# Kernel tuning notes

Measured on AMD Instinct MI355X. Metric: run time of the kernel, lower is better.

## Reference

```python
import jax, jax.numpy as jnp
import numpy as np

W, B, C, H = 1600, 4, 1, 900
DENSITY = 0.03          # fraction of valid radar returns per column
DEPTH_MAX = 80.0        # metric depth range


def setup_inputs() -> dict:
    key = jax.random.key(0)
    k1, k2, k3 = jax.random.split(key, 3)
    radar_depth = jax.random.uniform(k1, (W, B, C, H, 1), jnp.float32) * DEPTH_MAX + 1.0
    radar_mask = jax.random.uniform(k2, (W, B, C, H, 1), jnp.float32) < DENSITY
    radar_patches = jnp.where(radar_mask, radar_depth, 0.0)
    # dense monocular depth estimate, strictly positive (all 'valid')
    mde_out_patches = jax.random.uniform(k3, (W, B, C, H, 1), jnp.float32) * DEPTH_MAX + 1.0
    return {"radar_patches": radar_patches, "mde_out_patches": mde_out_patches}


def _process_column(radar_col, mde_col):
    """Sequentially place valid radar depths of one (w,b) column.

    radar_col, mde_col: [H] float (channel 0 of the column).
    Returns radar_gt column [H].
    Matches torch loop: for each valid radar y (ascending), pick mde row with
    closest depth (argmin |mde - d|, first index on ties); if that slot is
    already occupied, search outward offsets +1,-1,+2,-2,... for an empty slot;
    if none found, overwrite the best slot.
    """
    h = radar_col.shape[0]
    ys = jnp.arange(h)
    mde_valid = mde_col != 0
    has_mde = jnp.any(mde_valid)
    BIG = jnp.float32(1e30)
    KBIG = 4 * h  # sentinel key for occupied slots

    def step(col, y):
        depth = radar_col[y]
        valid = depth != 0
        # per-point argmin over valid mde depths
        diffs = jnp.where(mde_valid, jnp.abs(mde_col - depth), BIG)
        best_y = jnp.where(has_mde, jnp.argmin(diffs), y)
        # outward collision search as a vectorized argmin over a priority key:
        #   best_y itself -> 0; offset o, +dy before -dy -> 2*o + (dy<0)
        occ = col != 0
        dy = ys - best_y
        key = 2 * jnp.abs(dy) + (dy < 0).astype(jnp.int32)
        key = jnp.where(ys == best_y, 0, key)
        key = jnp.where(occ, KBIG, key)
        final_y = jnp.argmin(key)
        # all slots occupied -> fall back to best_y (torch overwrites there)
        final_y = jnp.where(key[final_y] >= KBIG, best_y, final_y)
        new_col = jnp.where(valid, col.at[final_y].set(depth), col)
        return new_col, None

    col, _ = jax.lax.scan(step, jnp.zeros(h, radar_col.dtype), ys)
    return col


def reference(radar_patches, mde_out_patches):
    # channel 0 only is read/written, as in the torch code
    radar0 = radar_patches[:, :, 0, :, 0]   # [W, B, H]
    mde0 = mde_out_patches[:, :, 0, :, 0]   # [W, B, H]
    cols = jax.vmap(jax.vmap(_process_column))(radar0, mde0)  # [W, B, H]
    w, b, h = cols.shape
    c = radar_patches.shape[2]
    radar_gt = jnp.zeros((b, c, h, w), radar_patches.dtype)
    radar_gt = radar_gt.at[:, 0].set(jnp.transpose(cols, (1, 2, 0)))  # [B, H, W]
    return radar_gt
```

## Files before the change

### kernel.cpp

```cpp
#include <hip/hip_runtime.h>
#include <cstdint>
#include <cstddef>

#define WDIM 1600
#define BDIM 4
#define HDIM 900
#define NV4  225
#define QCAP 96
#define KBIG (4 * HDIM)
#define BW   6

#define DPP_MINF(v, ctrl)                                                  \
    v = fminf(v, __int_as_float(__builtin_amdgcn_update_dpp(               \
            __float_as_int(v), __float_as_int(v), ctrl, 0xf, 0xf, false)))

__global__ __launch_bounds__(64) void radar_place_kernel(
    const float* __restrict__ radar, const float* __restrict__ mde,
    float* __restrict__ colout , int direct, float* __restrict__ out)
{
    __shared__ __align__(16) float s_col[HDIM];
    __shared__ float s_qd[QCAP];
    __shared__ int   s_qy[QCAP];

    const int lane = threadIdx.x;
    const int colid = blockIdx.x;
    const float4* mde4   = (const float4*)mde   + (long)colid * NV4;
    const float4* radar4 = (const float4*)radar + (long)colid * NV4;
    float4* col4 = (float4*)s_col;

    const unsigned long long below = (1ull << lane) - 1ull;

    bool hm = false;
#pragma unroll
    for (int c = 0; c < 4; ++c) {
        int i4 = c * 64 + lane;
        if (i4 < NV4) {
            float4 mv = mde4[i4];
            hm = hm || (mv.x != 0.f) || (mv.y != 0.f) || (mv.z != 0.f) || (mv.w != 0.f);
            col4[i4] = mv;
        }
    }
    const bool has_mde = (__ballot(hm) != 0ull);

    int Q = 0;
#pragma unroll
    for (int c = 0; c < 4; ++c) {
        int i4 = c * 64 + lane;
        bool in = (i4 < NV4);
        float4 rv = in ? radar4[i4] : make_float4(0.f, 0.f, 0.f, 0.f);
        unsigned long long b0 = __ballot(rv.x != 0.f);
        unsigned long long b1 = __ballot(rv.y != 0.f);
        unsigned long long b2 = __ballot(rv.z != 0.f);
        unsigned long long b3 = __ballot(rv.w != 0.f);
        int pos = Q + __popcll(b0 & below) + __popcll(b1 & below)
                    + __popcll(b2 & below) + __popcll(b3 & below);
        int y0 = i4 * 4;
        if (rv.x != 0.f) { if (pos < QCAP) { s_qd[pos] = rv.x; s_qy[pos] = y0;     } pos++; }
        if (rv.y != 0.f) { if (pos < QCAP) { s_qd[pos] = rv.y; s_qy[pos] = y0 + 1; } pos++; }
        if (rv.z != 0.f) { if (pos < QCAP) { s_qd[pos] = rv.z; s_qy[pos] = y0 + 2; } pos++; }
        if (rv.w != 0.f) { if (pos < QCAP) { s_qd[pos] = rv.w; s_qy[pos] = y0 + 3; } pos++; }
        Q += __popcll(b0) + __popcll(b1) + __popcll(b2) + __popcll(b3);
    }
    if (Q > QCAP) Q = QCAP;

    __syncthreads();

    float m[15];
    if (lane < 60) {
        int yb = lane * 15;
#pragma unroll
        for (int k = 0; k < 15; ++k) {
            float v = s_col[yb + k];
            m[k] = (v != 0.f) ? v : 1e30f;
        }
    } else {
#pragma unroll
        for (int k = 0; k < 15; ++k) m[k] = 1e30f;
    }

    __syncthreads();

#pragma unroll
    for (int c = 0; c < 4; ++c) {
        int i4 = c * 64 + lane;
        if (i4 < NV4) col4[i4] = make_float4(0.f, 0.f, 0.f, 0.f);
    }

    unsigned occ = (lane >= 60) ? 0x7FFFu : 0u;

    for (int t = 0; t < Q; t += BW) {
        float d[BW];
#pragma unroll
        for (int i = 0; i < BW; ++i) {
            int idx = (t + i < Q) ? (t + i) : (Q - 1);
            d[i] = s_qd[idx];
        }
        float bd[BW], bo[BW];
        int bik[BW];
#pragma unroll
        for (int i = 0; i < BW; ++i) { bd[i] = 3.4e38f; bik[i] = 0; }
#pragma unroll
        for (int k = 0; k < 15; ++k) {
            float mm = m[k];
#pragma unroll
            for (int i = 0; i < BW; ++i) {
                float af = fabsf(mm - d[i]);
                if (af < bd[i]) { bd[i] = af; bik[i] = k; }
            }
        }
#pragma unroll
        for (int i = 0; i < BW; ++i) bo[i] = bd[i];
#pragma unroll
        for (int i = 0; i < BW; ++i) DPP_MINF(bd[i], 0x111);
#pragma unroll
        for (int i = 0; i < BW; ++i) DPP_MINF(bd[i], 0x112);
#pragma unroll
        for (int i = 0; i < BW; ++i) DPP_MINF(bd[i], 0x114);
#pragma unroll
        for (int i = 0; i < BW; ++i) DPP_MINF(bd[i], 0x118);
#pragma unroll
        for (int i = 0; i < BW; ++i) DPP_MINF(bd[i], 0x142);
#pragma unroll
        for (int i = 0; i < BW; ++i) DPP_MINF(bd[i], 0x143);

#pragma unroll
        for (int i = 0; i < BW; ++i) {
            if (t + i < Q) {
                int best;
                if (has_mde) {
                    float gm = __int_as_float(
                        __builtin_amdgcn_readlane(__float_as_int(bd[i]), 63));
                    unsigned long long wm = __ballot(bo[i] == gm);
                    int win = __ffsll((long long)wm) - 1;
                    int kst = __shfl(bik[i], win);
                    best = win * 15 + kst;
                } else {
                    best = s_qy[t + i];
                }
                float depth = d[i];
                int sb = __builtin_amdgcn_readfirstlane(best);
                int bl = sb / 15, bk = sb % 15;
                unsigned long long bm = __ballot((occ >> bk) & 1u);
                int final_y = sb;
                if ((bm >> bl) & 1ull) {
                    int ko = 0x7fffffff, kk = 0;
#pragma unroll
                    for (int k = 0; k < 15; ++k) {
                        int yy = lane * 15 + k;
                        int o = (occ >> k) & 1;
                        int dy = yy - sb;
                        int ad = dy < 0 ? -dy : dy;
                        int key = o ? KBIG : (2 * ad + (dy < 0 ? 1 : 0));
                        if (key < ko) { ko = key; kk = k; }
                    }
                    int kmin = ko;
#pragma unroll
                    for (int off = 32; off; off >>= 1) {
                        int v = __shfl_xor(kmin, off);
                        kmin = (v < kmin) ? v : kmin;
                    }
                    if (kmin < KBIG) {
                        unsigned long long wm2 = __ballot(ko == kmin);
                        int w2 = __ffsll((long long)wm2) - 1;
                        int k2 = __shfl(kk, w2);
                        final_y = w2 * 15 + k2;
                    }
                }
                int sf = __builtin_amdgcn_readfirstlane(final_y);
                int fl = sf / 15, fk = sf % 15;
                if (lane == fl) occ |= (1u << fk);
                if (lane == 0) s_col[sf] = depth;
            }
        }
    }

    __syncthreads();

    if (direct) {
        int w_ = colid >> 2, b_ = colid & 3;
#pragma unroll
        for (int c = 0; c < 4; ++c) {
            int i4 = c * 64 + lane;
            if (i4 < NV4) {
                float4 v = col4[i4];
                int y = i4 * 4;
                out[((long)(b_ * HDIM + y + 0)) * WDIM + w_] = v.x;
                out[((long)(b_ * HDIM + y + 1)) * WDIM + w_] = v.y;
                out[((long)(b_ * HDIM + y + 2)) * WDIM + w_] = v.z;
                out[((long)(b_ * HDIM + y + 3)) * WDIM + w_] = v.w;
            }
        }
    } else {
        float4* colout4 = (float4*)colout + (long)colid * NV4;
#pragma unroll
        for (int c = 0; c < 4; ++c) {
            int i4 = c * 64 + lane;
            if (i4 < NV4) colout4[i4] = col4[i4];
        }
    }
}

__global__ __launch_bounds__(256) void transpose_kernel(
    const float* __restrict__ colout, float* __restrict__ out)
{
    __shared__ float tile[32][33];
    const int b  = blockIdx.z;
    const int h0 = blockIdx.x * 32;
    const int w0 = blockIdx.y * 32;
    const int tx = threadIdx.x & 31;
    const int ty = threadIdx.x >> 5;
#pragma unroll
    for (int j = 0; j < 4; ++j) {
        int wl = ty + j * 8;
        int w = w0 + wl;
        int h = h0 + tx;
        float v = 0.0f;
        if (h < HDIM && w < WDIM) v = colout[((long)(w * BDIM + b)) * HDIM + h];
        tile[wl][tx] = v;
    }
    __syncthreads();
#pragma unroll
    for (int j = 0; j < 4; ++j) {
        int hl = ty + j * 8;
        int h = h0 + hl;
        int w = w0 + tx;
        if (h < HDIM && w < WDIM)
            out[((long)(b * HDIM + h)) * WDIM + w] = tile[tx][hl];
    }
}

extern "C" void kernel_launch(void* const* d_in, const int* in_sizes, int n_in,
                              void* d_out, int out_size, void* d_ws, size_t ws_size,
                              hipStream_t stream) {
    const float* radar = (const float*)d_in[0];
    const float* mde   = (const float*)d_in[1];
    float* out = (float*)d_out;
    float* ws  = (float*)d_ws;

    const size_t need = (size_t)WDIM * BDIM * HDIM * sizeof(float);
    const int direct = (ws_size < need) ? 1 : 0;

    hipLaunchKernelGGL(radar_place_kernel,
                       dim3(WDIM * BDIM), dim3(64), 0, stream,
                       radar, mde, ws, direct, out);

    if (!direct) {
        dim3 g((HDIM + 31) / 32, WDIM / 32, BDIM);
        hipLaunchKernelGGL(transpose_kernel, g, dim3(256), 0, stream, ws, out);
    }
}
```

Before: 137.0 us.

## Pack four columns per block and decouple argmin from serial slot placement

Each block now runs four wavefronts, one column each, with per-wave shared buffers, and the block-wide barriers are removed. The radar queue is held in registers and broadcast with readlane instead of being reread from LDS. All best-row argmins are computed first in batches, then a separate serial loop resolves slot collisions using a DPP integer min-reduction instead of shfl_xor. Final depths are scattered in parallel by each owning lane. This cuts per-step latency in the serial placement chain and the launch/occupancy overhead of 64-thread blocks. The risk is that in the all-occupied fallback, where several points may write the same slot, the write order is no longer guaranteed.

```diff
diff --git a/kernel.cpp b/kernel.cpp
--- a/kernel.cpp
+++ b/kernel.cpp
@@ -9,24 +9,37 @@
 #define QCAP 96
 #define KBIG (4 * HDIM)
 #define BW   6
+#define NWAVE 4
 
 #define DPP_MINF(v, ctrl)                                                  \
     v = fminf(v, __int_as_float(__builtin_amdgcn_update_dpp(               \
             __float_as_int(v), __float_as_int(v), ctrl, 0xf, 0xf, false)))
-
-__global__ __launch_bounds__(64) void radar_place_kernel(
+#define DPP_MINI(v, ctrl)                                                  \
+    { int _t = __builtin_amdgcn_update_dpp(v, v, ctrl, 0xf, 0xf, false);   \
+      v = _t < v ? _t : v; }
+
+__device__ __forceinline__ float rdlane_f(float v, int l) {
+    return __int_as_float(__builtin_amdgcn_readlane(__float_as_int(v), l));
+}
+
+__global__ __launch_bounds__(64 * NWAVE, 6) void radar_place_kernel(
     const float* __restrict__ radar, const float* __restrict__ mde,
     float* __restrict__ colout , int direct, float* __restrict__ out)
 {
-    __shared__ __align__(16) float s_col[HDIM];
-    __shared__ float s_qd[QCAP];
-    __shared__ int   s_qy[QCAP];
-
-    const int lane = threadIdx.x;
-    const int colid = blockIdx.x;
+    __shared__ __align__(16) float s_col[NWAVE][HDIM];
+    __shared__ float s_qd[NWAVE][QCAP];
+    __shared__ int   s_qy[NWAVE][QCAP];
+
+    const int wave = threadIdx.x >> 6;
+    const int lane = threadIdx.x & 63;
+    const int colid = blockIdx.x * NWAVE + wave;
     const float4* mde4   = (const float4*)mde   + (long)colid * NV4;
     const float4* radar4 = (const float4*)radar + (long)colid * NV4;
-    float4* col4 = (float4*)s_col;
+
+    float*  colw = s_col[wave];
+    float4* col4 = (float4*)colw;
+    float*  qd   = s_qd[wave];
+    int*    qy   = s_qy[wave];
 
     const unsigned long long below = (1ull << lane) - 1ull;
 
@@ -55,22 +68,20 @@
         int pos = Q + __popcll(b0 & below) + __popcll(b1 & below)
                     + __popcll(b2 & below) + __popcll(b3 & below);
         int y0 = i4 * 4;
-        if (rv.x != 0.f) { if (pos < QCAP) { s_qd[pos] = rv.x; s_qy[pos] = y0;     } pos++; }
-        if (rv.y != 0.f) { if (pos < QCAP) { s_qd[pos] = rv.y; s_qy[pos] = y0 + 1; } pos++; }
-        if (rv.z != 0.f) { if (pos < QCAP) { s_qd[pos] = rv.z; s_qy[pos] = y0 + 2; } pos++; }
-        if (rv.w != 0.f) { if (pos < QCAP) { s_qd[pos] = rv.w; s_qy[pos] = y0 + 3; } pos++; }
+        if (rv.x != 0.f) { if (pos < QCAP) { qd[pos] = rv.x; qy[pos] = y0;     } pos++; }
+        if (rv.y != 0.f) { if (pos < QCAP) { qd[pos] = rv.y; qy[pos] = y0 + 1; } pos++; }
+        if (rv.z != 0.f) { if (pos < QCAP) { qd[pos] = rv.z; qy[pos] = y0 + 2; } pos++; }
+        if (rv.w != 0.f) { if (pos < QCAP) { qd[pos] = rv.w; qy[pos] = y0 + 3; } pos++; }
         Q += __popcll(b0) + __popcll(b1) + __popcll(b2) + __popcll(b3);
     }
     if (Q > QCAP) Q = QCAP;
-
-    __syncthreads();
 
     float m[15];
     if (lane < 60) {
         int yb = lane * 15;
 #pragma unroll
         for (int k = 0; k < 15; ++k) {
-            float v = s_col[yb + k];
+            float v = colw[yb + k];
             m[k] = (v != 0.f) ? v : 1e30f;
         }
     } else {
@@ -78,7 +89,10 @@
         for (int k = 0; k < 15; ++k) m[k] = 1e30f;
     }
 
-    __syncthreads();
+    float dq_lo = 0.f, dq_hi = 0.f;
+    int   qy_lo = 0,   qy_hi = 0;
+    if (lane < Q)      { dq_lo = qd[lane];      qy_lo = qy[lane]; }
+    if (lane + 64 < Q) { dq_hi = qd[lane + 64]; qy_hi = qy[lane + 64]; }
 
 #pragma unroll
     for (int c = 0; c < 4; ++c) {
@@ -86,14 +100,16 @@
         if (i4 < NV4) col4[i4] = make_float4(0.f, 0.f, 0.f, 0.f);
     }
 
-    unsigned occ = (lane >= 60) ? 0x7FFFu : 0u;
-
+    int best_lo = 0, best_hi = 0;
     for (int t = 0; t < Q; t += BW) {
+        int idxs[BW];
         float d[BW];
 #pragma unroll
         for (int i = 0; i < BW; ++i) {
-            int idx = (t + i < Q) ? (t + i) : (Q - 1);
-            d[i] = s_qd[idx];
+            int idx = t + i; if (idx >= Q) idx = Q - 1;
+            idxs[i] = idx;
+            if (idx < 64) d[i] = rdlane_f(dq_lo, idx);
+            else          d[i] = rdlane_f(dq_hi, idx - 64);
         }
         float bd[BW], bo[BW];
         int bik[BW];
@@ -122,59 +138,71 @@
         for (int i = 0; i < BW; ++i) DPP_MINF(bd[i], 0x142);
 #pragma unroll
         for (int i = 0; i < BW; ++i) DPP_MINF(bd[i], 0x143);
-
 #pragma unroll
         for (int i = 0; i < BW; ++i) {
-            if (t + i < Q) {
-                int best;
-                if (has_mde) {
-                    float gm = __int_as_float(
-                        __builtin_amdgcn_readlane(__float_as_int(bd[i]), 63));
-                    unsigned long long wm = __ballot(bo[i] == gm);
-                    int win = __ffsll((long long)wm) - 1;
-                    int kst = __shfl(bik[i], win);
-                    best = win * 15 + kst;
-                } else {
-                    best = s_qy[t + i];
-                }
-                float depth = d[i];
-                int sb = __builtin_amdgcn_readfirstlane(best);
-                int bl = sb / 15, bk = sb % 15;
-                unsigned long long bm = __ballot((occ >> bk) & 1u);
-                int final_y = sb;
-                if ((bm >> bl) & 1ull) {
-                    int ko = 0x7fffffff, kk = 0;
-#pragma unroll
-                    for (int k = 0; k < 15; ++k) {
-                        int yy = lane * 15 + k;
-                        int o = (occ >> k) & 1;
-                        int dy = yy - sb;
-                        int ad = dy < 0 ? -dy : dy;
-                        int key = o ? KBIG : (2 * ad + (dy < 0 ? 1 : 0));
-                        if (key < ko) { ko = key; kk = k; }
-                    }
-                    int kmin = ko;
-#pragma unroll
-                    for (int off = 32; off; off >>= 1) {
-                        int v = __shfl_xor(kmin, off);
-                        kmin = (v < kmin) ? v : kmin;
-                    }
-                    if (kmin < KBIG) {
-                        unsigned long long wm2 = __ballot(ko == kmin);
-                        int w2 = __ffsll((long long)wm2) - 1;
-                        int k2 = __shfl(kk, w2);
-                        final_y = w2 * 15 + k2;
-                    }
-                }
-                int sf = __builtin_amdgcn_readfirstlane(final_y);
-                int fl = sf / 15, fk = sf % 15;
-                if (lane == fl) occ |= (1u << fk);
-                if (lane == 0) s_col[sf] = depth;
-            }
-        }
-    }
-
-    __syncthreads();
+            int idx = idxs[i];
+            int sb;
+            if (has_mde) {
+                float gm = rdlane_f(bd[i], 63);
+                unsigned long long wm = __ballot(bo[i] == gm);
+                int win = __ffsll((long long)wm) - 1;
+                int kst = __builtin_amdgcn_readlane(bik[i], win);
+                sb = win * 15 + kst;
+            } else {
+                if (idx < 64) sb = __builtin_amdgcn_readlane(qy_lo, idx);
+                else          sb = __builtin_amdgcn_readlane(qy_hi, idx - 64);
+            }
+            if (idx < 64) { if (lane == idx)      best_lo = sb; }
+            else          { if (lane == idx - 64) best_hi = sb; }
+        }
+    }
+
+    unsigned occ = (lane >= 60) ? 0x7FFFu : 0u;
+    int fy_lo = 0, fy_hi = 0;
+
+    auto place_one = [&](int sb) -> int {
+        int bl = sb / 15, bk = sb - bl * 15;
+        unsigned long long bm = __ballot((occ >> bk) & 1u);
+        int fy = sb;
+        if ((bm >> bl) & 1ull) {
+            int ko = 0x7fffffff, kk = 0;
+#pragma unroll
+            for (int k = 0; k < 15; ++k) {
+                int yy = lane * 15 + k;
+                int o = (occ >> k) & 1;
+                int dy = yy - sb;
+                int ad = dy < 0 ? -dy : dy;
+                int key = o ? KBIG : (2 * ad + (dy < 0 ? 1 : 0));
+                if (key < ko) { ko = key; kk = k; }
+            }
+            int km = ko;
+            DPP_MINI(km, 0x111); DPP_MINI(km, 0x112); DPP_MINI(km, 0x114);
+            DPP_MINI(km, 0x118); DPP_MINI(km, 0x142); DPP_MINI(km, 0x143);
+            int gkm = __builtin_amdgcn_readlane(km, 63);
+            if (gkm < KBIG) {
+                unsigned long long wm2 = __ballot(ko == gkm);
+                int w2 = __ffsll((long long)wm2) - 1;
+                int k2 = __builtin_amdgcn_readlane(kk, w2);
+                fy = w2 * 15 + k2;
+            }
+        }
+        int fl2 = fy / 15, fk2 = fy - (fy / 15) * 15;
+        if (lane == fl2) occ |= (1u << fk2);
+        return fy;
+    };
+
+    int Qlo = Q < 64 ? Q : 64;
+    for (int q = 0; q < Qlo; ++q) {
+        int fy = place_one(__builtin_amdgcn_readlane(best_lo, q));
+        if (lane == q) fy_lo = fy;
+    }
+    for (int q = 64; q < Q; ++q) {
+        int fy = place_one(__builtin_amdgcn_readlane(best_hi, q - 64));
+        if (lane == q - 64) fy_hi = fy;
+    }
+
+    if (lane < Q)      colw[fy_lo] = dq_lo;
+    if (lane + 64 < Q) colw[fy_hi] = dq_hi;
 
     if (direct) {
         int w_ = colid >> 2, b_ = colid & 3;
@@ -241,7 +269,7 @@
     const int direct = (ws_size < need) ? 1 : 0;
 
     hipLaunchKernelGGL(radar_place_kernel,
-                       dim3(WDIM * BDIM), dim3(64), 0, stream,
+                       dim3(WDIM * BDIM / NWAVE), dim3(64 * NWAVE), 0, stream,
                        radar, mde, ws, direct, out);
 
     if (!direct) {
```

Measured after the change: 138.7 us. About the same (+1.2%).
